# Performance work log

Hardware: AMD Instinct MI355X
Metric: run time of the kernel (lower is better)

Reference implementation:

```python
import jax, jax.numpy as jnp
import numpy as np

T, B, IN, H, OUT = 345, 128, 13, 128, 9

# snnTorch ATan surrogate spike: forward = heaviside(x), backward = 1/(1+(pi*x)^2) (alpha=2)
@jax.custom_vjp
def spike_fn(x):
    return (x > 0).astype(x.dtype)

def _spike_fwd(x):
    return spike_fn(x), x

def _spike_bwd(x, g):
    return (g / (1.0 + (jnp.pi * x) ** 2),)

spike_fn.defvjp(_spike_fwd, _spike_bwd)


def setup_inputs() -> dict:
    key = jax.random.key(0)
    ks = jax.random.split(key, 5)
    x = jax.random.normal(ks[0], (B, IN, T), dtype=jnp.float32)
    # PyTorch Linear init: U(-1/sqrt(fan_in), 1/sqrt(fan_in))
    lim1 = 1.0 / np.sqrt(IN)
    lim2 = 1.0 / np.sqrt(H)
    W1 = jax.random.uniform(ks[1], (H, IN), minval=-lim1, maxval=lim1, dtype=jnp.float32)
    b1 = jax.random.uniform(ks[2], (H,), minval=-lim1, maxval=lim1, dtype=jnp.float32)
    W2 = jax.random.uniform(ks[3], (OUT, H), minval=-lim2, maxval=lim2, dtype=jnp.float32)
    b2 = jax.random.uniform(ks[4], (OUT,), minval=-lim2, maxval=lim2, dtype=jnp.float32)
    beta1 = jnp.float32(0.9)
    thr1 = jnp.float32(1.0)
    beta2 = jnp.float32(0.9)
    thr2 = jnp.float32(1.0)
    return {"x": x, "W1": W1, "b1": b1, "W2": W2, "b2": b2,
            "beta1": beta1, "thr1": thr1, "beta2": beta2, "thr2": thr2}


def reference(x, W1, b1, W2, b2, beta1, thr1, beta2, thr2):
    # Precompute fc1 for all steps: (T, B, H)
    cur1_all = jnp.einsum('bct,hc->tbh', x, W1) + b1
    bt1 = jnp.clip(beta1, 0.0, 1.0)
    bt2 = jnp.clip(beta2, 0.0, 1.0)

    def step(carry, cur1):
        mem1, mem2 = carry
        mem1 = bt1 * mem1 + cur1                 # leaky integrate
        spk1 = spike_fn(mem1 - thr1)             # fire
        mem1 = mem1 - spk1 * thr1                # subtract reset
        cur2 = spk1 @ W2.T + b2                  # (B, OUT)
        mem2 = bt2 * mem2 + cur2
        spk2 = spike_fn(mem2 - thr2)
        mem2 = mem2 - spk2 * thr2
        return (mem1, mem2), (spk2, mem2)

    init = (jnp.zeros((B, H), x.dtype), jnp.zeros((B, OUT), x.dtype))
    _, (spk_rec, mem_rec) = jax.lax.scan(step, init, cur1_all)
    return spk_rec, mem_rec  # each (T, B, OUT)
```

## Files before the change

### kernel.cpp

```cpp
#include <hip/hip_runtime.h>

#define T_STEPS 345
#define B_SZ    128
#define IN_SZ   13
#define H_SZ    128
#define OUT_SZ  9
#define XT      348
#define CPAD    388
#define NBO     (B_SZ * OUT_SZ)
#define CHUNK   92
#define BUFR    104


__device__ __forceinline__ void emit_rows(float* __restrict__ buf,
                                          const float* __restrict__ xs,
                                          const float (&w1r)[IN_SZ], float b1r,
                                          int T0, int L, int h, int off, int stride)
{
    int tl = off;
    for (; tl + stride < L; tl += 2 * stride) {
        const int ta = T0 + tl, tb = T0 + tl + stride;
        float ca = b1r, cb = b1r;
#pragma unroll
        for (int c = 0; c < IN_SZ; ++c) {
            ca = fmaf(xs[c * XT + ta], w1r[c], ca);
            cb = fmaf(xs[c * XT + tb], w1r[c], cb);
        }
        buf[tl * H_SZ + h] = ca;
        buf[(tl + stride) * H_SZ + h] = cb;
    }
    if (tl < L) {
        const int ta = T0 + tl;
        float ca = b1r;
#pragma unroll
        for (int c = 0; c < IN_SZ; ++c) ca = fmaf(xs[c * XT + ta], w1r[c], ca);
        buf[tl * H_SZ + h] = ca;
    }
}

__device__ __forceinline__ void scan1_step(float& mem1, float u, float bt1, float th1,
                                           unsigned long long* __restrict__ msh,
                                           int t, bool sl, int half)
{
    mem1 = fmaf(bt1, mem1, u);
    const bool p = mem1 > th1;
    const unsigned long long m = __ballot(p);
    const float ms = mem1 - th1;
    mem1 = p ? ms : mem1;
    if (sl) msh[t * 2 + half] = m;
}

__device__ __forceinline__ void scan1_chunk(const float* __restrict__ buf,
                                            unsigned long long* __restrict__ msh,
                                            int T0, int L, int h,
                                            float bt1, float th1, float& mem1)
{
    const float* cb = buf + h;
    const bool sl = (h & 63) == 0;
    const int half = h >> 6;
    float a0 = cb[0*128], a1 = cb[1*128], a2 = cb[ 2*128], a3 = cb[ 3*128];
    float b0 = cb[4*128], b1v= cb[5*128], b2v= cb[ 6*128], b3 = cb[ 7*128];
    float c0 = cb[8*128], c1v= cb[9*128], c2v= cb[10*128], c3 = cb[11*128];
    const int fullg = L >> 2;
    const int rem   = L & 3;
    for (int g = 0; g < fullg; ++g) {
        const float u0 = a0, u1 = a1, u2 = a2, u3 = a3;
        a0 = b0; a1 = b1v; a2 = b2v; a3 = b3;
        b0 = c0; b1v = c1v; b2v = c2v; b3 = c3;
        const float* nb = cb + (g + 3) * 4 * 128;
        c0 = nb[0]; c1v = nb[128]; c2v = nb[256]; c3 = nb[384];
        const int tb = T0 + g * 4;
        scan1_step(mem1, u0, bt1, th1, msh, tb + 0, sl, half);
        scan1_step(mem1, u1, bt1, th1, msh, tb + 1, sl, half);
        scan1_step(mem1, u2, bt1, th1, msh, tb + 2, sl, half);
        scan1_step(mem1, u3, bt1, th1, msh, tb + 3, sl, half);
    }
    const int tb = T0 + fullg * 4;
    if (rem > 0) scan1_step(mem1, a0, bt1, th1, msh, tb + 0, sl, half);
    if (rem > 1) scan1_step(mem1, a1, bt1, th1, msh, tb + 1, sl, half);
    if (rem > 2) scan1_step(mem1, a2, bt1, th1, msh, tb + 2, sl, half);
}

__global__ __launch_bounds__(1024, 1)
void snn_fused(const float* __restrict__ x, const float* __restrict__ W1,
               const float* __restrict__ b1, const float* __restrict__ W2,
               const float* __restrict__ b2,
               const float* __restrict__ beta1p, const float* __restrict__ thr1p,
               const float* __restrict__ beta2p, const float* __restrict__ thr2p,
               float* __restrict__ out)
{
    const int b    = blockIdx.x >> 1;
    const int half = blockIdx.x & 1;
    const int tid  = threadIdx.x;
    const int wid  = tid >> 6;
    const int lane = tid & 63;
    const int hown = tid & 127;
    const int jsl  = tid >> 7;

    __shared__ __align__(16) float xst[IN_SZ * XT];
    __shared__ __align__(16) float cur1s[2][BUFR * H_SZ];
    __shared__ __align__(16) unsigned long long msh[352 * 2];
    __shared__ __align__(16) float c2s[OUT_SZ * CPAD];

    const float bt1 = fminf(fmaxf(beta1p[0], 0.0f), 1.0f);
    const float th1 = thr1p[0];
    const float bt2 = fminf(fmaxf(beta2p[0], 0.0f), 1.0f);
    const float th2 = thr2p[0];

    const float* xb = x + (size_t)b * (IN_SZ * T_STEPS);
    for (int i = tid; i < IN_SZ * T_STEPS; i += 1024) {
        const int c = i / T_STEPS;
        const int t = i - c * T_STEPS;
        xst[c * XT + t] = xb[i];
    }
    float* W1t = c2s;
    for (int i = tid; i < IN_SZ * H_SZ; i += 1024) {
        const int h = i / IN_SZ;
        const int c = i - IN_SZ * h;
        W1t[c * H_SZ + h] = W1[i];
    }
    __syncthreads();

    float w1r[IN_SZ];
#pragma unroll
    for (int c = 0; c < IN_SZ; ++c) w1r[c] = W1t[c * H_SZ + hown];
    const float b1r = b1[hown];

    emit_rows(cur1s[0], xst, w1r, b1r, 0, CHUNK, hown, jsl, 8);
    __syncthreads();

    float mem1 = 0.0f;
    for (int k = 0; k < 4; ++k) {
        if (tid < 128) {
            const int L = (k < 3) ? CHUNK : (T_STEPS - 3 * CHUNK);
            scan1_chunk(cur1s[k & 1], msh, k * CHUNK, L, tid, bt1, th1, mem1);
        } else if (k < 3) {
            const int kn = k + 1;
            const int L = (kn < 3) ? CHUNK : (T_STEPS - 3 * CHUNK);
            emit_rows(cur1s[kn & 1], xst, w1r, b1r, kn * CHUNK, L, hown, jsl - 1, 7);
        }
        __syncthreads();
    }

    const int obase  = half ? 5 : 0;
    const int ntasks = half ? 4 : 5;

    float mem2 = 0.0f;
    const int o_sc = obase + lane;
    float* out_spk = out + (size_t)b * OUT_SZ + o_sc;
    float* out_mem = out_spk + (size_t)T_STEPS * NBO;
    const float4* src4 = (const float4*)(c2s + lane * CPAD);

    for (int s = 0; s < 6; ++s) {
        if (wid < 7) {
            if (wid < ntasks) {
                const int o = obase + wid;
                const int t = s * 64 + lane;
                const int tc = (t < T_STEPS) ? t : (T_STEPS - 1);
                const uint4 mm = *(const uint4*)((const char*)msh + (size_t)tc * 16);
                const float* __restrict__ w2row = W2 + o * H_SZ;
                float acc = 0.0f;
#pragma unroll
                for (int h = 0; h < 32; ++h)
                    acc = fmaf((float)((mm.x >> h) & 1u), w2row[h], acc);
#pragma unroll
                for (int h = 0; h < 32; ++h)
                    acc = fmaf((float)((mm.y >> h) & 1u), w2row[32 + h], acc);
#pragma unroll
                for (int h = 0; h < 32; ++h)
                    acc = fmaf((float)((mm.z >> h) & 1u), w2row[64 + h], acc);
#pragma unroll
                for (int h = 0; h < 32; ++h)
                    acc = fmaf((float)((mm.w >> h) & 1u), w2row[96 + h], acc);
                c2s[wid * CPAD + t] = acc + b2[o];
            }
        } else if (wid == 7 && s > 0 && lane < ntasks) {
            const int sb = (s - 1) * 16;
            float4 fA = src4[sb], fB = src4[sb + 1];
#pragma unroll
            for (int i = 0; i < 16; ++i) {
                const float4 u = fA; fA = fB; fB = src4[sb + i + 2];
                const float vv[4] = { u.x, u.y, u.z, u.w };
#pragma unroll
                for (int kk = 0; kk < 4; ++kk) {
                    const int tt = (s - 1) * 64 + i * 4 + kk;
                    mem2 = fmaf(bt2, mem2, vv[kk]);
                    const bool p = mem2 > th2;
                    const float s2 = p ? 1.0f : 0.0f;
                    const float ms = mem2 - th2;
                    mem2 = p ? ms : mem2;
                    out_spk[(size_t)tt * NBO] = s2;
                    out_mem[(size_t)tt * NBO] = mem2;
                }
            }
        }
        __syncthreads();
    }

    if (wid == 7 && lane < ntasks) {
        const int sb = 5 * 16;
        float4 fA = src4[sb], fB = src4[sb + 1];
#pragma unroll
        for (int i = 0; i < 16; ++i) {
            const float4 u = fA; fA = fB; fB = src4[sb + i + 2];
            const float vv[4] = { u.x, u.y, u.z, u.w };
#pragma unroll
            for (int kk = 0; kk < 4; ++kk) {
                const int tt = 5 * 64 + i * 4 + kk;
                if (tt < T_STEPS) {
                    mem2 = fmaf(bt2, mem2, vv[kk]);
                    const bool p = mem2 > th2;
                    const float s2 = p ? 1.0f : 0.0f;
                    const float ms = mem2 - th2;
                    mem2 = p ? ms : mem2;
                    out_spk[(size_t)tt * NBO] = s2;
                    out_mem[(size_t)tt * NBO] = mem2;
                }
            }
        }
    }
}

extern "C" void kernel_launch(void* const* d_in, const int* in_sizes, int n_in,
                              void* d_out, int out_size, void* d_ws, size_t ws_size,
                              hipStream_t stream) {
    const float* x     = (const float*)d_in[0];
    const float* W1    = (const float*)d_in[1];
    const float* b1    = (const float*)d_in[2];
    const float* W2    = (const float*)d_in[3];
    const float* b2    = (const float*)d_in[4];
    const float* beta1 = (const float*)d_in[5];
    const float* thr1  = (const float*)d_in[6];
    const float* beta2 = (const float*)d_in[7];
    const float* thr2  = (const float*)d_in[8];
    float* out = (float*)d_out;
    (void)in_sizes; (void)n_in; (void)out_size; (void)d_ws; (void)ws_size;

    snn_fused<<<dim3(B_SZ * 2), dim3(1024), 0, stream>>>(
        x, W1, b1, W2, b2, beta1, thr1, beta2, thr2, out);
}
```

Before: 103.5 us.

## Overlap first cur2 chunk with scan1 and widen layer-2 pipeline stages

Idle warps during the scan1 phase now start the layer-2 current (spike times W2) computation for the first 128 timesteps. The layer-2 stage is restructured into 128-step chunks computed by up to 10 warps (two time halves per output), with a single warp running the mem2 scan one chunk behind. This drops from six barrier-separated stages plus a tail to three. The cost is more concurrent warps contending for W2 loads, and a longer serial scan per stage.

```diff
diff --git a/kernel.cpp b/kernel.cpp
--- a/kernel.cpp
+++ b/kernel.cpp
@@ -81,6 +81,62 @@
     if (rem > 2) scan1_step(mem1, a2, bt1, th1, msh, tb + 2, sl, half);
 }
 
+__device__ __forceinline__ void cur2_task(int j, int tb, int obase, int lane,
+                                          const unsigned long long* __restrict__ msh,
+                                          const float* __restrict__ W2,
+                                          const float* __restrict__ b2,
+                                          float* __restrict__ c2s)
+{
+    const int o_l = j >> 1;
+    const int o_u = __builtin_amdgcn_readfirstlane(obase + o_l);
+    const int t   = tb + ((j & 1) << 6) + lane;
+    const int tc  = (t < T_STEPS) ? t : (T_STEPS - 1);
+    const uint4 mm = *(const uint4*)((const char*)msh + (size_t)tc * 16);
+    const float* __restrict__ w2row = W2 + o_u * H_SZ;
+    float acc = 0.0f;
+#pragma unroll
+    for (int h = 0; h < 32; ++h)
+        acc = fmaf((float)((mm.x >> h) & 1u), w2row[h], acc);
+#pragma unroll
+    for (int h = 0; h < 32; ++h)
+        acc = fmaf((float)((mm.y >> h) & 1u), w2row[32 + h], acc);
+#pragma unroll
+    for (int h = 0; h < 32; ++h)
+        acc = fmaf((float)((mm.z >> h) & 1u), w2row[64 + h], acc);
+#pragma unroll
+    for (int h = 0; h < 32; ++h)
+        acc = fmaf((float)((mm.w >> h) & 1u), w2row[96 + h], acc);
+    c2s[(o_u - obase) * CPAD + t] = acc + b2[o_u];
+}
+
+template<bool TAIL>
+__device__ __forceinline__ void scan2_chunk(const float4* __restrict__ src4, int ci,
+                                            float bt2, float th2, float& mem2,
+                                            float* __restrict__ out_spk,
+                                            float* __restrict__ out_mem)
+{
+    const int sb = ci * 32;
+    float4 fA = src4[sb], fB = src4[sb + 1];
+#pragma unroll
+    for (int i = 0; i < 32; ++i) {
+        const float4 u = fA; fA = fB; fB = src4[sb + i + 2];
+        const float vv[4] = { u.x, u.y, u.z, u.w };
+#pragma unroll
+        for (int kk = 0; kk < 4; ++kk) {
+            const int tt = ci * 128 + i * 4 + kk;
+            if (!TAIL || tt < T_STEPS) {
+                mem2 = fmaf(bt2, mem2, vv[kk]);
+                const bool p = mem2 > th2;
+                const float s2 = p ? 1.0f : 0.0f;
+                const float ms = mem2 - th2;
+                mem2 = p ? ms : mem2;
+                out_spk[(size_t)tt * NBO] = s2;
+                out_mem[(size_t)tt * NBO] = mem2;
+            }
+        }
+    }
+}
+
 __global__ __launch_bounds__(1024, 1)
 void snn_fused(const float* __restrict__ x, const float* __restrict__ W1,
                const float* __restrict__ b1, const float* __restrict__ W2,
@@ -125,6 +181,10 @@
 #pragma unroll
     for (int c = 0; c < IN_SZ; ++c) w1r[c] = W1t[c * H_SZ + hown];
     const float b1r = b1[hown];
+
+    const int obase  = half ? 5 : 0;
+    const int ntasks = half ? 4 : 5;
+    const int NT2    = ntasks * 2;
 
     emit_rows(cur1s[0], xst, w1r, b1r, 0, CHUNK, hown, jsl, 8);
     __syncthreads();
@@ -138,12 +198,12 @@
             const int kn = k + 1;
             const int L = (kn < 3) ? CHUNK : (T_STEPS - 3 * CHUNK);
             emit_rows(cur1s[kn & 1], xst, w1r, b1r, kn * CHUNK, L, hown, jsl - 1, 7);
+        } else {
+            const int j = wid - 2;
+            if (j < NT2) cur2_task(j, 0, obase, lane, msh, W2, b2, c2s);
         }
         __syncthreads();
     }
-
-    const int obase  = half ? 5 : 0;
-    const int ntasks = half ? 4 : 5;
 
     float mem2 = 0.0f;
     const int o_sc = obase + lane;
@@ -151,73 +211,22 @@
     float* out_mem = out_spk + (size_t)T_STEPS * NBO;
     const float4* src4 = (const float4*)(c2s + lane * CPAD);
 
-    for (int s = 0; s < 6; ++s) {
-        if (wid < 7) {
-            if (wid < ntasks) {
-                const int o = obase + wid;
-                const int t = s * 64 + lane;
-                const int tc = (t < T_STEPS) ? t : (T_STEPS - 1);
-                const uint4 mm = *(const uint4*)((const char*)msh + (size_t)tc * 16);
-                const float* __restrict__ w2row = W2 + o * H_SZ;
-                float acc = 0.0f;
-#pragma unroll
-                for (int h = 0; h < 32; ++h)
-                    acc = fmaf((float)((mm.x >> h) & 1u), w2row[h], acc);
-#pragma unroll
-                for (int h = 0; h < 32; ++h)
-                    acc = fmaf((float)((mm.y >> h) & 1u), w2row[32 + h], acc);
-#pragma unroll
-                for (int h = 0; h < 32; ++h)
-                    acc = fmaf((float)((mm.z >> h) & 1u), w2row[64 + h], acc);
-#pragma unroll
-                for (int h = 0; h < 32; ++h)
-                    acc = fmaf((float)((mm.w >> h) & 1u), w2row[96 + h], acc);
-                c2s[wid * CPAD + t] = acc + b2[o];
-            }
-        } else if (wid == 7 && s > 0 && lane < ntasks) {
-            const int sb = (s - 1) * 16;
-            float4 fA = src4[sb], fB = src4[sb + 1];
-#pragma unroll
-            for (int i = 0; i < 16; ++i) {
-                const float4 u = fA; fA = fB; fB = src4[sb + i + 2];
-                const float vv[4] = { u.x, u.y, u.z, u.w };
-#pragma unroll
-                for (int kk = 0; kk < 4; ++kk) {
-                    const int tt = (s - 1) * 64 + i * 4 + kk;
-                    mem2 = fmaf(bt2, mem2, vv[kk]);
-                    const bool p = mem2 > th2;
-                    const float s2 = p ? 1.0f : 0.0f;
-                    const float ms = mem2 - th2;
-                    mem2 = p ? ms : mem2;
-                    out_spk[(size_t)tt * NBO] = s2;
-                    out_mem[(size_t)tt * NBO] = mem2;
-                }
-            }
-        }
-        __syncthreads();
-    }
-
-    if (wid == 7 && lane < ntasks) {
-        const int sb = 5 * 16;
-        float4 fA = src4[sb], fB = src4[sb + 1];
-#pragma unroll
-        for (int i = 0; i < 16; ++i) {
-            const float4 u = fA; fA = fB; fB = src4[sb + i + 2];
-            const float vv[4] = { u.x, u.y, u.z, u.w };
-#pragma unroll
-            for (int kk = 0; kk < 4; ++kk) {
-                const int tt = 5 * 64 + i * 4 + kk;
-                if (tt < T_STEPS) {
-                    mem2 = fmaf(bt2, mem2, vv[kk]);
-                    const bool p = mem2 > th2;
-                    const float s2 = p ? 1.0f : 0.0f;
-                    const float ms = mem2 - th2;
-                    mem2 = p ? ms : mem2;
-                    out_spk[(size_t)tt * NBO] = s2;
-                    out_mem[(size_t)tt * NBO] = mem2;
-                }
-            }
-        }
+    if (wid < 15) {
+        if (wid < NT2) cur2_task(wid, 128, obase, lane, msh, W2, b2, c2s);
+    } else if (lane < ntasks) {
+        scan2_chunk<false>(src4, 0, bt2, th2, mem2, out_spk, out_mem);
+    }
+    __syncthreads();
+
+    if (wid < 15) {
+        if (wid < NT2) cur2_task(wid, 256, obase, lane, msh, W2, b2, c2s);
+    } else if (lane < ntasks) {
+        scan2_chunk<false>(src4, 1, bt2, th2, mem2, out_spk, out_mem);
+    }
+    __syncthreads();
+
+    if (wid == 15 && lane < ntasks) {
+        scan2_chunk<true>(src4, 2, bt2, th2, mem2, out_spk, out_mem);
     }
 }
 
```

Result: slower. 108.2 us (+4.5%).
